# Kernel tuning notes

Measured on AMD Instinct MI355X. Metric: run time of the kernel, lower is better.

The kernel has to match this reference:

```python
import jax, jax.numpy as jnp
import numpy as np

# NF4 codebook (bitsandbytes normal-float-4 quantile values)
NF4 = jnp.array([-1.0, -0.6961928009986877, -0.5250730514526367, -0.39491748809814453,
                 -0.28444138169288635, -0.18477343022823334, -0.09105003625154495, 0.0,
                 0.07958029955625534, 0.16093020141124725, 0.24611230194568634,
                 0.33791524171829224, 0.44070982933044434, 0.5626170039176941,
                 0.7229568362236023, 1.0], dtype=jnp.float32)
BLOCK = 64          # bnb default quantization block size
SCALING = 32.0 / 16.0  # lora_alpha / r


def setup_inputs() -> dict:
    key = jax.random.key(0)
    k1, k2, k3, k4, k5 = jax.random.split(key, 5)
    B, S, DIN, DOUT, R = 4, 2048, 4096, 4096, 16
    x = jax.random.normal(k1, (B, S, DIN), dtype=jnp.float32)
    w_codes = jax.random.randint(k2, (DOUT, DIN), 0, 16, dtype=jnp.int32)
    absmax = jax.random.uniform(k3, (DOUT, DIN // BLOCK), dtype=jnp.float32)
    lora_A_w = jax.random.normal(k4, (R, DIN), dtype=jnp.float32) * (1.0 / np.sqrt(DIN))
    lora_B_w = jax.random.normal(k5, (DOUT, R), dtype=jnp.float32) * 0.02
    return {"x": x, "w_codes": w_codes, "absmax": absmax,
            "lora_A_w": lora_A_w, "lora_B_w": lora_B_w}


def _dequant_nf4(w_codes, absmax):
    # codes -> codebook values, scaled per contiguous block of BLOCK elements per row
    dout, din = w_codes.shape
    w = NF4[w_codes].reshape(dout, din // BLOCK, BLOCK) * absmax[:, :, None]
    return w.reshape(dout, din)  # [out, in] float32


def reference(x, w_codes, absmax, lora_A_w, lora_B_w):
    w = _dequant_nf4(w_codes, absmax)                      # [out, in]
    logits = jnp.einsum('bsd,od->bso', x, w)               # base 4-bit path
    a = jnp.einsum('bsd,rd->bsr', x, lora_A_w)             # [b,s,r]
    lora = jnp.einsum('bsr,or->bso', a, lora_B_w) * SCALING
    return logits + lora
```

## Files before the change

kernel.cpp:

```cpp
#include <hip/hip_runtime.h>

#define GLOBAL_AS __attribute__((address_space(1)))
#define LDS_AS    __attribute__((address_space(3)))

typedef short bf16x8 __attribute__((ext_vector_type(8)));
typedef float f32x4  __attribute__((ext_vector_type(4)));

#define M_DIM 8192
#define N_DIM 4096
#define K_DIM 4096
#define R_DIM 16

__constant__ float NF4C[16] = {
    -1.0f, -0.6961928009986877f, -0.5250730514526367f, -0.39491748809814453f,
    -0.28444138169288635f, -0.18477343022823334f, -0.09105003625154495f, 0.0f,
    0.07958029955625534f, 0.16093020141124725f, 0.24611230194568634f,
    0.33791524171829224f, 0.44070982933044434f, 0.5626170039176941f,
    0.7229568362236023f, 1.0f};

__device__ __forceinline__ unsigned short f2bf(float f) {
    unsigned int u = __float_as_uint(f);
    u += 0x7fffu + ((u >> 16) & 1u);
    return (unsigned short)(u >> 16);
}

__global__ __launch_bounds__(256) void prep_x_kernel(
        const float4* __restrict__ x4, unsigned short* __restrict__ xb) {
    const int idx = blockIdx.x * 256 + threadIdx.x;
    float4 v = x4[idx];
    ushort4 o;
    o.x = f2bf(v.x); o.y = f2bf(v.y); o.z = f2bf(v.z); o.w = f2bf(v.w);
    *(ushort4*)(xb + (size_t)idx * 4) = o;
}

__global__ __launch_bounds__(256) void dequant_kernel(
        const int4* __restrict__ codes4, const float* __restrict__ absmax,
        const float4* __restrict__ loraB4, const float4* __restrict__ A4,
        unsigned short* __restrict__ wq) {
    const int idx = blockIdx.x * 256 + threadIdx.x;
    const int n = idx >> 10;
    const int k4 = idx & 1023;
    const float am = absmax[n * 64 + (k4 >> 4)];
    int4 c = codes4[idx];
    float4 b[4];
#pragma unroll
    for (int j = 0; j < 4; ++j) b[j] = loraB4[n * 4 + j];
    float bax = 0.f, bay = 0.f, baz = 0.f, baw = 0.f;
#pragma unroll
    for (int r = 0; r < 16; ++r) {
        const float br = (r & 2) ? ((r & 1) ? b[r >> 2].w : b[r >> 2].z)
                                 : ((r & 1) ? b[r >> 2].y : b[r >> 2].x);
        float4 av = A4[r * 1024 + k4];
        bax += br * av.x; bay += br * av.y; baz += br * av.z; baw += br * av.w;
    }
    ushort4 o;
    o.x = f2bf(NF4C[c.x] * am + 2.0f * bax);
    o.y = f2bf(NF4C[c.y] * am + 2.0f * bay);
    o.z = f2bf(NF4C[c.z] * am + 2.0f * baz);
    o.w = f2bf(NF4C[c.w] * am + 2.0f * baw);
    *(ushort4*)(wq + (size_t)n * K_DIM + k4 * 4) = o;
}

#define STG(gptr, ldsoff)                                                   \
    __builtin_amdgcn_global_load_lds((const GLOBAL_AS void*)(gptr),         \
                                     (LDS_AS void*)(smem + (ldsoff)), 16, 0, 0)
#define STAGE_A(d, kh, kt) do {                                             \
    STG(gA + (size_t)(kt) * 64 + (kh) * 32,                                 \
        (d) * 16384 + (kh) * 8192 + wave * 512);                            \
    STG(gA + (size_t)128 * K_DIM + (size_t)(kt) * 64 + (kh) * 32,           \
        (d) * 16384 + (kh) * 8192 + 4096 + wave * 512); } while (0)
#define STAGE_B(d, kh, kt) do {                                             \
    STG(gB + (size_t)(kt) * 64 + (kh) * 32,                                 \
        32768 + (d) * 16384 + (kh) * 8192 + wave * 512);                    \
    STG(gB + (size_t)128 * K_DIM + (size_t)(kt) * 64 + (kh) * 32,           \
        32768 + (d) * 16384 + (kh) * 8192 + 4096 + wave * 512); } while (0)
#define NOPX ((void)0)
#define VMCNT6 asm volatile("s_waitcnt vmcnt(6)" ::: "memory")
#define VMCNT0 asm volatile("s_waitcnt vmcnt(0)" ::: "memory")

#define PHASE(d, kh, mig, STAGE_STMT, VM_STMT) do {                         \
    bf16x8 af[4];                                                           \
    _Pragma("unroll")                                                       \
    for (int i_ = 0; i_ < 4; ++i_)                                          \
        af[i_] = *(const bf16x8*)(smem + (d) * 16384 + (kh) * 8192 + aoff + \
                                  ((mig) * 4 + i_) * 512);                  \
    if ((mig) == 0) {                                                       \
        _Pragma("unroll")                                                   \
        for (int j_ = 0; j_ < 4; ++j_)                                      \
            bfr[j_] = *(const bf16x8*)(smem + (d) * 16384 + (kh) * 8192 +   \
                                       boff + j_ * 512);                    \
    }                                                                       \
    STAGE_STMT;                                                             \
    __builtin_amdgcn_s_barrier();                                           \
    asm volatile("s_waitcnt lgkmcnt(0)" ::: "memory");                      \
    __builtin_amdgcn_sched_barrier(0);                                      \
    __builtin_amdgcn_s_setprio(1);                                          \
    _Pragma("unroll")                                                       \
    for (int i_ = 0; i_ < 4; ++i_)                                          \
        _Pragma("unroll")                                                   \
        for (int j_ = 0; j_ < 4; ++j_)                                      \
            acc[(mig) * 4 + i_][j_] = __builtin_amdgcn_mfma_f32_16x16x32_bf16( \
                af[i_], bfr[j_], acc[(mig) * 4 + i_][j_], 0, 0, 0);         \
    __builtin_amdgcn_s_setprio(0);                                          \
    VM_STMT;                                                                \
    __builtin_amdgcn_s_barrier();                                           \
} while (0)

__global__ __launch_bounds__(512) void gemm_kernel(
        const unsigned short* __restrict__ xb,
        const unsigned short* __restrict__ wq,
        float* __restrict__ out) {
    __shared__ __align__(16) unsigned short smem[65536];
    const int tid = threadIdx.x;
    const int wave = tid >> 6, lane = tid & 63;

    const int bid = blockIdx.y * 16 + blockIdx.x;
    const int swz = (bid & 7) * 64 + (bid >> 3);
    const int m0 = (swz >> 4) * 256;
    const int n0 = (swz & 15) * 256;

    const int schunk = ((lane & 3) ^ ((lane >> 3) & 3)) * 8;
    const unsigned short* gA =
        xb + (size_t)(m0 + wave * 16 + (lane >> 2)) * K_DIM + schunk;
    const unsigned short* gB =
        wq + (size_t)(n0 + wave * 16 + (lane >> 2)) * K_DIM + schunk;

    const int wr = wave >> 2, wc = wave & 3;
    const int fm = lane & 15, q = lane >> 4;
    const int rk = (q ^ ((fm >> 1) & 3)) * 8;
    const int aoff = wr * 4096 + fm * 32 + rk;
    const int boff = 32768 + wc * 2048 + fm * 32 + rk;

    f32x4 acc[8][4] = {};
    bf16x8 bfr[4];

    STAGE_A(0, 0, 0); STAGE_B(0, 0, 0); STAGE_A(0, 1, 0); STAGE_B(0, 1, 0);
    STAGE_B(1, 0, 1); STAGE_A(1, 0, 1); STAGE_B(1, 1, 1);
    VMCNT6;
    __builtin_amdgcn_s_barrier();

#pragma unroll 1
    for (int kt = 0; kt < 62; kt += 2) {
        PHASE(0, 0, 0, STAGE_A(1, 1, kt + 1), NOPX);
        PHASE(0, 0, 1, STAGE_B(0, 0, kt + 2), NOPX);
        PHASE(0, 1, 0, STAGE_A(0, 0, kt + 2), NOPX);
        PHASE(0, 1, 1, STAGE_B(0, 1, kt + 2), VMCNT6);
        PHASE(1, 0, 0, STAGE_A(0, 1, kt + 2), NOPX);
        PHASE(1, 0, 1, STAGE_B(1, 0, kt + 3), NOPX);
        PHASE(1, 1, 0, STAGE_A(1, 0, kt + 3), NOPX);
        PHASE(1, 1, 1, STAGE_B(1, 1, kt + 3), VMCNT6);
    }
    PHASE(0, 0, 0, STAGE_A(1, 1, 63), NOPX);
    PHASE(0, 0, 1, NOPX, NOPX);
    PHASE(0, 1, 0, NOPX, NOPX);
    PHASE(0, 1, 1, NOPX, VMCNT0);
    PHASE(1, 0, 0, NOPX, NOPX);
    PHASE(1, 0, 1, NOPX, NOPX);
    PHASE(1, 1, 0, NOPX, NOPX);
    PHASE(1, 1, 1, NOPX, NOPX);

    const int col0 = n0 + wc * 64 + fm;
    const int row0 = m0 + wr * 128 + q * 4;
#pragma unroll
    for (int mi = 0; mi < 8; ++mi)
#pragma unroll
        for (int ni = 0; ni < 4; ++ni)
#pragma unroll
            for (int r = 0; r < 4; ++r)
                out[(size_t)(row0 + mi * 16 + r) * N_DIM + col0 + ni * 16] =
                    acc[mi][ni][r];
}

extern "C" void kernel_launch(void* const* d_in, const int* in_sizes, int n_in,
                              void* d_out, int out_size, void* d_ws, size_t ws_size,
                              hipStream_t stream) {
    const float* x      = (const float*)d_in[0];
    const int*   codes  = (const int*)d_in[1];
    const float* absmax = (const float*)d_in[2];
    const float* loraA  = (const float*)d_in[3];
    const float* loraB  = (const float*)d_in[4];
    float* out = (float*)d_out;

    unsigned short* xb = (unsigned short*)d_ws;
    unsigned short* wq = xb + (size_t)M_DIM * K_DIM;

    prep_x_kernel<<<(M_DIM * K_DIM / 4) / 256, 256, 0, stream>>>(
        (const float4*)x, xb);
    dequant_kernel<<<(N_DIM * K_DIM / 4) / 256, 256, 0, stream>>>(
        (const int4*)codes, absmax, (const float4*)loraB, (const float4*)loraA, wq);

    dim3 grid(N_DIM / 256, M_DIM / 256);
    gemm_kernel<<<grid, 512, 0, stream>>>(xb, wq, out);
}
```

Baseline: 545.4 us.

## Switch GEMM to 32x32x16 MFMA and merge prep kernels into one launch

Replaces the 16x16x32 bf16 MFMA tiling with 32x32x16 MFMA, changing the LDS fragment addressing, accumulator layout and output store mapping. The larger MFMA shape cuts the number of LDS fragment reads per FLOP. Separately, the x-conversion and weight-dequant kernels are fused into a single launch whose blocks branch by index. This saves one kernel launch, but a wrong swizzle or accumulator row mapping would produce incorrect results.

```diff
diff --git a/kernel.cpp b/kernel.cpp
--- a/kernel.cpp
+++ b/kernel.cpp
@@ -5,6 +5,7 @@
 
 typedef short bf16x8 __attribute__((ext_vector_type(8)));
 typedef float f32x4  __attribute__((ext_vector_type(4)));
+typedef float f32x16 __attribute__((ext_vector_type(16)));
 
 #define M_DIM 8192
 #define N_DIM 4096
@@ -24,20 +25,25 @@
     return (unsigned short)(u >> 16);
 }
 
-__global__ __launch_bounds__(256) void prep_x_kernel(
-        const float4* __restrict__ x4, unsigned short* __restrict__ xb) {
-    const int idx = blockIdx.x * 256 + threadIdx.x;
-    float4 v = x4[idx];
-    ushort4 o;
-    o.x = f2bf(v.x); o.y = f2bf(v.y); o.z = f2bf(v.z); o.w = f2bf(v.w);
-    *(ushort4*)(xb + (size_t)idx * 4) = o;
-}
-
-__global__ __launch_bounds__(256) void dequant_kernel(
-        const int4* __restrict__ codes4, const float* __restrict__ absmax,
-        const float4* __restrict__ loraB4, const float4* __restrict__ A4,
+__global__ __launch_bounds__(256) void prep_kernel(
+        const float4* __restrict__ x4, const int4* __restrict__ codes4,
+        const float* __restrict__ absmax, const float4* __restrict__ loraB4,
+        const float4* __restrict__ A4, unsigned short* __restrict__ xb,
         unsigned short* __restrict__ wq) {
-    const int idx = blockIdx.x * 256 + threadIdx.x;
+    const int tid = threadIdx.x;
+    if (blockIdx.x >= 16384) {
+        const int b = blockIdx.x - 16384;
+#pragma unroll
+        for (int j = 0; j < 4; ++j) {
+            const int idx = b * 1024 + j * 256 + tid;
+            float4 v = x4[idx];
+            ushort4 o;
+            o.x = f2bf(v.x); o.y = f2bf(v.y); o.z = f2bf(v.z); o.w = f2bf(v.w);
+            *(ushort4*)(xb + (size_t)idx * 4) = o;
+        }
+        return;
+    }
+    const int idx = blockIdx.x * 256 + tid;
     const int n = idx >> 10;
     const int k4 = idx & 1023;
     const float am = absmax[n * 64 + (k4 >> 4)];
@@ -79,16 +85,21 @@
 #define VMCNT0 asm volatile("s_waitcnt vmcnt(0)" ::: "memory")
 
 #define PHASE(d, kh, mig, STAGE_STMT, VM_STMT) do {                         \
-    bf16x8 af[4];                                                           \
+    const int rb_ = (d) * 16384 + (kh) * 8192;                              \
+    bf16x8 af_[2][2];                                                       \
     _Pragma("unroll")                                                       \
-    for (int i_ = 0; i_ < 4; ++i_)                                          \
-        af[i_] = *(const bf16x8*)(smem + (d) * 16384 + (kh) * 8192 + aoff + \
-                                  ((mig) * 4 + i_) * 512);                  \
+    for (int mi_ = 0; mi_ < 2; ++mi_) {                                     \
+        const int a0_ = rb_ + aoff + ((mig) * 2 + mi_) * 1024;              \
+        af_[mi_][0] = *(const bf16x8*)(smem + a0_);                         \
+        af_[mi_][1] = *(const bf16x8*)(smem + (a0_ ^ 16));                  \
+    }                                                                       \
     if ((mig) == 0) {                                                       \
         _Pragma("unroll")                                                   \
-        for (int j_ = 0; j_ < 4; ++j_)                                      \
-            bfr[j_] = *(const bf16x8*)(smem + (d) * 16384 + (kh) * 8192 +   \
-                                       boff + j_ * 512);                    \
+        for (int ni_ = 0; ni_ < 2; ++ni_) {                                 \
+            const int b0_ = rb_ + boff + ni_ * 1024;                        \
+            bfr[ni_][0] = *(const bf16x8*)(smem + b0_);                     \
+            bfr[ni_][1] = *(const bf16x8*)(smem + (b0_ ^ 16));              \
+        }                                                                   \
     }                                                                       \
     STAGE_STMT;                                                             \
     __builtin_amdgcn_s_barrier();                                           \
@@ -96,11 +107,15 @@
     __builtin_amdgcn_sched_barrier(0);                                      \
     __builtin_amdgcn_s_setprio(1);                                          \
     _Pragma("unroll")                                                       \
-    for (int i_ = 0; i_ < 4; ++i_)                                          \
+    for (int ks_ = 0; ks_ < 2; ++ks_)                                       \
         _Pragma("unroll")                                                   \
-        for (int j_ = 0; j_ < 4; ++j_)                                      \
-            acc[(mig) * 4 + i_][j_] = __builtin_amdgcn_mfma_f32_16x16x32_bf16( \
-                af[i_], bfr[j_], acc[(mig) * 4 + i_][j_], 0, 0, 0);         \
+        for (int mi_ = 0; mi_ < 2; ++mi_)                                   \
+            _Pragma("unroll")                                               \
+            for (int ni_ = 0; ni_ < 2; ++ni_)                               \
+                acc[(mig) * 2 + mi_][ni_] =                                 \
+                    __builtin_amdgcn_mfma_f32_32x32x16_bf16(                \
+                        af_[mi_][ks_], bfr[ni_][ks_],                       \
+                        acc[(mig) * 2 + mi_][ni_], 0, 0, 0);                \
     __builtin_amdgcn_s_setprio(0);                                          \
     VM_STMT;                                                                \
     __builtin_amdgcn_s_barrier();                                           \
@@ -126,13 +141,13 @@
         wq + (size_t)(n0 + wave * 16 + (lane >> 2)) * K_DIM + schunk;
 
     const int wr = wave >> 2, wc = wave & 3;
-    const int fm = lane & 15, q = lane >> 4;
-    const int rk = (q ^ ((fm >> 1) & 3)) * 8;
-    const int aoff = wr * 4096 + fm * 32 + rk;
-    const int boff = 32768 + wc * 2048 + fm * 32 + rk;
-
-    f32x4 acc[8][4] = {};
-    bf16x8 bfr[4];
+    const int l31 = lane & 31, c0 = lane >> 5;
+    const int key = (l31 >> 1) & 3;
+    const int aoff = (wr * 128 + l31) * 32 + ((c0 ^ key) * 8);
+    const int boff = 32768 + (wc * 64 + l31) * 32 + ((c0 ^ key) * 8);
+
+    f32x16 acc[4][2] = {};
+    bf16x8 bfr[2][2];
 
     STAGE_A(0, 0, 0); STAGE_B(0, 0, 0); STAGE_A(0, 1, 0); STAGE_B(0, 1, 0);
     STAGE_B(1, 0, 1); STAGE_A(1, 0, 1); STAGE_B(1, 1, 1);
@@ -159,16 +174,17 @@
     PHASE(1, 1, 0, NOPX, NOPX);
     PHASE(1, 1, 1, NOPX, NOPX);
 
-    const int col0 = n0 + wc * 64 + fm;
-    const int row0 = m0 + wr * 128 + q * 4;
-#pragma unroll
-    for (int mi = 0; mi < 8; ++mi)
-#pragma unroll
-        for (int ni = 0; ni < 4; ++ni)
-#pragma unroll
-            for (int r = 0; r < 4; ++r)
-                out[(size_t)(row0 + mi * 16 + r) * N_DIM + col0 + ni * 16] =
-                    acc[mi][ni][r];
+    const int col0 = n0 + wc * 64 + l31;
+    const int row0 = m0 + wr * 128 + c0 * 4;
+#pragma unroll
+    for (int mi = 0; mi < 4; ++mi)
+#pragma unroll
+        for (int ni = 0; ni < 2; ++ni)
+#pragma unroll
+            for (int r = 0; r < 16; ++r) {
+                const int row = row0 + mi * 32 + (r & 3) + 8 * (r >> 2);
+                out[(size_t)row * N_DIM + col0 + ni * 32] = acc[mi][ni][r];
+            }
 }
 
 extern "C" void kernel_launch(void* const* d_in, const int* in_sizes, int n_in,
@@ -184,10 +200,9 @@
     unsigned short* xb = (unsigned short*)d_ws;
     unsigned short* wq = xb + (size_t)M_DIM * K_DIM;
 
-    prep_x_kernel<<<(M_DIM * K_DIM / 4) / 256, 256, 0, stream>>>(
-        (const float4*)x, xb);
-    dequant_kernel<<<(N_DIM * K_DIM / 4) / 256, 256, 0, stream>>>(
-        (const int4*)codes, absmax, (const float4*)loraB, (const float4*)loraA, wq);
+    prep_kernel<<<24576, 256, 0, stream>>>(
+        (const float4*)x, (const int4*)codes, absmax, (const float4*)loraB,
+        (const float4*)loraA, xb, wq);
 
     dim3 grid(N_DIM / 256, M_DIM / 256);
     gemm_kernel<<<grid, 512, 0, stream>>>(xb, wq, out);
```

Result: slower. 562.6 us (+3.1%).
